# Optimization experiments

Hardware: AMD Instinct MI355X
Metric: run time of the kernel (lower is better)

The kernel has to match this reference:

```python
import jax, jax.numpy as jnp
import numpy as np

HIDDEN = 2048
KEY_DIM = 2048
NUM_HEADS = 16
HEAD_DIM = KEY_DIM // NUM_HEADS
ROPE_THETA = 10000.0
EPS = 1e-05


def rms_norm(x, w, eps=EPS):
    var = jnp.mean(x * x, axis=-1, keepdims=True)
    return x * jax.lax.rsqrt(var + eps) * w


def apply_rope(x, theta_base=ROPE_THETA):
    # x: [b, s, h, d]; faithful to the einops repeat '(2 d)' = tile (concat), with
    # even output positions = cos*x1 - sin*x2, odd = sin*x1 + cos*x2.
    b, s, h, d = x.shape
    half = d // 2
    freqs = theta_base ** (jnp.arange(half, dtype=x.dtype) * (-2.0 / d))  # [d/2]
    freqs = jnp.concatenate([freqs, freqs], axis=-1)                      # [d] (tiled)
    pos = jnp.arange(s, dtype=x.dtype)                                    # [s]
    ang = pos[:, None] * freqs[None, :]                                   # [s, d]
    cos = jnp.cos(ang)[None, :, None, :]
    sin = jnp.sin(ang)[None, :, None, :]
    x_even = x[..., 0::2]
    x_odd = x[..., 1::2]
    x1 = jnp.concatenate([x_even, x_even], axis=-1)  # tile '(2 d)'
    x2 = jnp.concatenate([x_odd, x_odd], axis=-1)
    even_mask = (jnp.arange(d) % 2 == 0)[None, None, None, :]
    return jnp.where(even_mask, cos * x1 - sin * x2, sin * x1 + cos * x2)


def setup_inputs() -> dict:
    key = jax.random.key(0)
    ks = jax.random.split(key, 10)
    B, S = 2, 2048
    s_in = 1.0 / np.sqrt(HIDDEN)
    s_k = 1.0 / np.sqrt(KEY_DIM)
    return {
        "x": jax.random.normal(ks[0], (B, S, HIDDEN), dtype=jnp.float32),
        "rms_w": jnp.ones((HIDDEN,), dtype=jnp.float32),
        "wq": jax.random.normal(ks[1], (HIDDEN, KEY_DIM), dtype=jnp.float32) * s_in,
        "bq": jnp.zeros((KEY_DIM,), dtype=jnp.float32),
        "wk": jax.random.normal(ks[2], (HIDDEN, KEY_DIM), dtype=jnp.float32) * s_in,
        "bk": jnp.zeros((KEY_DIM,), dtype=jnp.float32),
        "wv": jax.random.normal(ks[3], (HIDDEN, KEY_DIM), dtype=jnp.float32) * s_in,
        "bv": jnp.zeros((KEY_DIM,), dtype=jnp.float32),
        "wo": jax.random.normal(ks[4], (KEY_DIM, HIDDEN), dtype=jnp.float32) * s_k,
        "bo": jnp.zeros((HIDDEN,), dtype=jnp.float32),
    }


def reference(x, rms_w, wq, bq, wk, bk, wv, bv, wo, bo):
    B, S, _ = x.shape
    residual = x
    xn = rms_norm(x, rms_w)
    q = (xn @ wq + bq).reshape(B, S, NUM_HEADS, HEAD_DIM)
    k = (xn @ wk + bk).reshape(B, S, NUM_HEADS, HEAD_DIM)
    v = (xn @ wv + bv).reshape(B, S, NUM_HEADS, HEAD_DIM)
    q = apply_rope(q)
    k = apply_rope(k)
    scores = jnp.einsum('bshd,bthd->bhst', q, k) / jnp.sqrt(
        jnp.asarray(HEAD_DIM, dtype=x.dtype))
    causal = jnp.tril(jnp.ones((S, S), dtype=bool))[None, None]
    scores = jnp.where(causal, scores, -jnp.inf)
    probs = jax.nn.softmax(scores, axis=-1)
    out = jnp.einsum('bhst,bthd->bshd', probs, v).reshape(B, S, KEY_DIM)
    return out @ wo + bo + residual
```

## Files before the change

### kernel.cpp

```cpp
#include <hip/hip_runtime.h>
#include <stdint.h>
#include <math.h>

#define S_LEN 2048
#define HID 2048
#define NH 16
#define HD 128
#define NROWS 4096
#define SCALE 0.08838834764831845f
#define C2 (0.08838834764831845f * 1.442695040888963f)

typedef unsigned short u16;
typedef __attribute__((ext_vector_type(8))) short short8;
typedef __attribute__((ext_vector_type(4))) float f32x4;
typedef __attribute__((ext_vector_type(16))) float f32x16;
typedef __attribute__((ext_vector_type(4))) unsigned short u16x4;
typedef __attribute__((ext_vector_type(4))) unsigned int u32x4;
typedef __attribute__((ext_vector_type(4))) float float4v;

__device__ __forceinline__ u16 f2bf(float f) {
  union { float f; uint32_t u; } v; v.f = f;
  uint32_t r = v.u + 0x7FFFu + ((v.u >> 16) & 1u);
  return (u16)(r >> 16);
}
__device__ __forceinline__ float bf2f(u16 b) {
  union { uint32_t u; float f; } v; v.u = ((uint32_t)b) << 16;
  return v.f;
}
__device__ __forceinline__ void gl_lds16(const void* g, void* l) {
  __builtin_amdgcn_global_load_lds((const __attribute__((address_space(1))) void*)g,
                                   (__attribute__((address_space(3))) void*)l, 16, 0, 0);
}
__device__ __forceinline__ unsigned cvtpk(float lo, float hi) {
  unsigned r;
  asm("v_cvt_pk_bf16_f32 %0, %1, %2" : "=v"(r) : "v"(lo), "v"(hi));
  return r;
}
__device__ __forceinline__ void plswap(unsigned &a, unsigned &b) {
  asm volatile("v_permlane32_swap_b32 %0, %1" : "+v"(a), "+v"(b));
}

__global__ __launch_bounds__(256) void k_pre(const float* __restrict__ x, const float* __restrict__ rw,
                                             u16* __restrict__ xn,
                                             const float* __restrict__ w0, const float* __restrict__ w1,
                                             const float* __restrict__ w2, const float* __restrict__ w3,
                                             u16* __restrict__ wtbase) {
  int bid = blockIdx.x;
  int tid = threadIdx.x;
  if (bid < 4096) {
    int row = bid;
    const float* xr = x + (size_t)row * HID;
    float4v a = *(const float4v*)(xr + tid * 8);
    float4v b = *(const float4v*)(xr + tid * 8 + 4);
    float s = a[0]*a[0] + a[1]*a[1] + a[2]*a[2] + a[3]*a[3]
            + b[0]*b[0] + b[1]*b[1] + b[2]*b[2] + b[3]*b[3];
    #pragma unroll
    for (int off = 1; off < 64; off <<= 1) s += __shfl_xor(s, off, 64);
    __shared__ float red[4];
    int wv = tid >> 6;
    if ((tid & 63) == 0) red[wv] = s;
    __syncthreads();
    float tot = red[0] + red[1] + red[2] + red[3];
    float r = rsqrtf(tot * (1.0f / HID) + 1e-5f);
    const float* wp = rw + tid * 8;
    u16x4 o0, o1;
    #pragma unroll
    for (int j = 0; j < 4; ++j) { o0[j] = f2bf(a[j] * r * wp[j]); o1[j] = f2bf(b[j] * r * wp[4 + j]); }
    *(u16x4*)(xn + (size_t)row * HID + tid * 8) = o0;
    *(u16x4*)(xn + (size_t)row * HID + tid * 8 + 4) = o1;
  } else {
    int c = bid - 4096;
    int z = c >> 10;
    int rest = c & 1023;
    int n0 = (rest & 31) * 64, k0 = (rest >> 5) * 64;
    const float* w = (z == 0) ? w0 : (z == 1) ? w1 : (z == 2) ? w2 : w3;
    u16* wt = wtbase + (size_t)z * HID * HID;
    __shared__ float t[64][68];
    int cr = tid >> 4;
    int cc = (tid & 15) * 4;
    #pragma unroll
    for (int it = 0; it < 4; ++it) {
      int kk = cr + it * 16;
      float4v v = *(const float4v*)(w + (size_t)(k0 + kk) * HID + n0 + cc);
      t[kk][cc] = v[0]; t[kk][cc + 1] = v[1]; t[kk][cc + 2] = v[2]; t[kk][cc + 3] = v[3];
    }
    __syncthreads();
    #pragma unroll
    for (int it = 0; it < 4; ++it) {
      int nn = cr + it * 16;
      u16x4 o;
      #pragma unroll
      for (int j = 0; j < 4; ++j) o[j] = f2bf(t[cc + j][nn]);
      *(u16x4*)(wt + (size_t)(n0 + nn) * HID + k0 + cc) = o;
    }
  }
}

__global__ __launch_bounds__(256) void k_post(const u16* __restrict__ qh, const u16* __restrict__ kh,
                                              u16* __restrict__ QP, u16* __restrict__ KP,
                                              const u16* __restrict__ vh, u16* __restrict__ VP) {
  int bid = blockIdx.x;
  int tid = threadIdx.x;
  if (bid < 4096) {
    int l = tid & 63, wvv = tid >> 6;
    int rsub = l >> 4, c = l & 15;
    int row = bid * 16 + wvv * 4 + rsub;
    int bh = row >> 11, s = row & 2047;
    int tile = s >> 5, ln = s & 31;
    int ks = c >> 1, hi = c & 1;
    int k3 = ks & 3;
    const u16* qi = qh + (size_t)row * HD + 32 * k3 + 16 * hi;
    const u16* ki = kh + (size_t)row * HD + 32 * k3 + 16 * hi;
    float sn[8], cs[8];
    #pragma unroll
    for (int j = 0; j < 8; ++j) {
      int de = 16 * k3 + 8 * hi + j;
      float freq = exp2f((float)de * -0.20762050593046014f);
      sincosf((float)s * freq, &sn[j], &cs[j]);
    }
    size_t off = ((((size_t)(bh * 64 + tile)) * 8 + ks) * 64 + hi * 32 + ln) * 8;
    {
      short8 a = *(const short8*)(qi);
      short8 b2 = *(const short8*)(qi + 8);
      u16x4 o0, o1;
      #pragma unroll
      for (int j = 0; j < 4; ++j) {
        float x0 = bf2f((u16)a[2 * j]), x1 = bf2f((u16)a[2 * j + 1]);
        o0[j] = f2bf((j & 1) ? (sn[j] * x0 + cs[j] * x1) : (cs[j] * x0 - sn[j] * x1));
      }
      #pragma unroll
      for (int j = 0; j < 4; ++j) {
        int jj = j + 4;
        float x0 = bf2f((u16)b2[2 * j]), x1 = bf2f((u16)b2[2 * j + 1]);
        o1[j] = f2bf((jj & 1) ? (sn[jj] * x0 + cs[jj] * x1) : (cs[jj] * x0 - sn[jj] * x1));
      }
      *(u16x4*)(QP + off) = o0; *(u16x4*)(QP + off + 4) = o1;
    }
    {
      short8 a = *(const short8*)(ki);
      short8 b2 = *(const short8*)(ki + 8);
      u16x4 o0, o1;
      #pragma unroll
      for (int j = 0; j < 4; ++j) {
        float x0 = bf2f((u16)a[2 * j]), x1 = bf2f((u16)a[2 * j + 1]);
        o0[j] = f2bf((j & 1) ? (sn[j] * x0 + cs[j] * x1) : (cs[j] * x0 - sn[j] * x1));
      }
      #pragma unroll
      for (int j = 0; j < 4; ++j) {
        int jj = j + 4;
        float x0 = bf2f((u16)b2[2 * j]), x1 = bf2f((u16)b2[2 * j + 1]);
        o1[j] = f2bf((jj & 1) ? (sn[jj] * x0 + cs[jj] * x1) : (cs[jj] * x0 - sn[jj] * x1));
      }
      *(u16x4*)(KP + off) = o0; *(u16x4*)(KP + off + 4) = o1;
    }
  } else {
    int c = bid - 4096;
    int bx = c & 31;
    int bh = c >> 5;
    __shared__ u16 t[64][136];
    int row = tid >> 2;
    int d0 = (tid & 3) * 32;
    const u16* src = vh + ((size_t)bh * S_LEN + bx * 64 + row) * HD + d0;
    short8 a = *(const short8*)(src);
    short8 b = *(const short8*)(src + 8);
    short8 cc2 = *(const short8*)(src + 16);
    short8 d = *(const short8*)(src + 24);
    *(short8*)(&t[row][d0]) = a;
    *(short8*)(&t[row][d0 + 8]) = b;
    *(short8*)(&t[row][d0 + 16]) = cc2;
    *(short8*)(&t[row][d0 + 24]) = d;
    __syncthreads();
    #pragma unroll
    for (int i = 0; i < 4; ++i) {
      int cid = i * 256 + tid;
      int lp = cid & 63;
      int db = (cid >> 6) & 3;
      int j2 = (cid >> 8) & 1;
      int tl = (cid >> 9) & 1;
      int tg = bx * 2 + tl;
      int tloc = tl * 32 + j2 * 16 + (lp >> 5) * 8;
      int dloc = db * 32 + (lp & 31);
      short8 v;
      #pragma unroll
      for (int jj = 0; jj < 8; ++jj) v[jj] = (short)t[tloc + jj][dloc];
      size_t off = ((((size_t)(bh * 64 + tg) * 2 + j2) * 4 + db) * 64 + lp) * 8;
      *(short8*)(VP + off) = v;
    }
  }
}

__global__ __launch_bounds__(512, 1) void k_gemm_qkv2(const u16* __restrict__ A, const u16* __restrict__ BT,
                                                      const float* __restrict__ bq, const float* __restrict__ bk,
                                                      const float* __restrict__ bv, u16* __restrict__ qkv) {
  extern __shared__ __align__(16) char smraw[];
  u16* sm = (u16*)smraw;
  int bid = blockIdx.x;
  int xcd = bid & 7, loc = bid >> 3;
  int bx = xcd * 3 + loc % 3;
  int by = loc / 3;
  int tid = threadIdx.x;
  int w = tid >> 6, lane = tid & 63;
  int wr = w >> 2, wc = w & 3;
  int lq = lane & 15, lg = lane >> 4;

  f32x4 acc[4][4];
  #pragma unroll
  for (int mi = 0; mi < 4; ++mi)
    #pragma unroll
    for (int ni = 0; ni < 4; ++ni) acc[mi][ni] = (f32x4){0.f, 0.f, 0.f, 0.f};

  const size_t Abase = (size_t)(by * 128) * HID;
  const size_t Bbase = (size_t)(bx * 256) * HID;

  #define STAGE_A(n)  do { \
    int slot_ = ((n) % 3) * 24576; \
    int kb_ = (n) * 64; \
    _Pragma("unroll") \
    for (int it_ = 0; it_ < 2; ++it_) { \
      int c_ = it_ * 512 + tid; int row_ = c_ >> 3; int cs_ = (c_ & 7) ^ (row_ & 7); \
      gl_lds16(A + Abase + (size_t)row_ * HID + kb_ + cs_ * 8, sm + slot_ + c_ * 8); } \
  } while (0)
  #define STAGE_B(n, h)  do { \
    int slot_ = ((n) % 3) * 24576; \
    int kb_ = (n) * 64; \
    _Pragma("unroll") \
    for (int it_ = 0; it_ < 2; ++it_) { \
      int c_ = it_ * 512 + tid; int row_ = c_ >> 3; int cs_ = (c_ & 7) ^ (row_ & 7); \
      gl_lds16(BT + Bbase + (size_t)(128 * (h) + row_) * HID + kb_ + cs_ * 8, \
               sm + slot_ + 8192 + 8192 * (h) + c_ * 8); } \
  } while (0)

  STAGE_A(0); STAGE_B(0, 0); STAGE_B(0, 1);
  STAGE_A(1); STAGE_B(1, 0); STAGE_B(1, 1);
  asm volatile("s_waitcnt vmcnt(6)" ::: "memory");
  __builtin_amdgcn_s_barrier();
  __builtin_amdgcn_sched_barrier(0);

  for (int t = 0; t < 32; ++t) {
    int slot = (t % 3) * 24576;
    const u16* sA = sm + slot;
    const u16* sB = sm + slot + 8192;
    if (t == 31) asm volatile("s_waitcnt vmcnt(0)" ::: "memory");
    else         asm volatile("s_waitcnt vmcnt(6)" ::: "memory");
    short8 af[4][2], bf0[2][2];
    #pragma unroll
    for (int mi = 0; mi < 4; ++mi) {
      int ra = wr * 64 + mi * 16 + lq;
      #pragma unroll
      for (int ks = 0; ks < 2; ++ks)
        af[mi][ks] = *(const short8*)(sA + ra * 64 + (((ks * 4 + lg) ^ (ra & 7)) << 3));
    }
    #pragma unroll
    for (int nl = 0; nl < 2; ++nl) {
      int rb = wc * 64 + nl * 16 + lq;
      #pragma unroll
      for (int ks = 0; ks < 2; ++ks)
        bf0[nl][ks] = *(const short8*)(sB + rb * 64 + (((ks * 4 + lg) ^ (rb & 7)) << 3));
    }
    if (t + 2 < 32) { STAGE_A(t + 2); STAGE_B(t + 2, 0); }
    __builtin_amdgcn_s_setprio(1);
    #pragma unroll
    for (int ks = 0; ks < 2; ++ks)
      #pragma unroll
      for (int mi = 0; mi < 4; ++mi)
        #pragma unroll
        for (int nl = 0; nl < 2; ++nl)
          acc[mi][nl] = __builtin_amdgcn_mfma_f32_16x16x32_bf16(af[mi][ks], bf0[nl][ks], acc[mi][nl], 0, 0, 0);
    __builtin_amdgcn_s_setprio(0);
    __builtin_amdgcn_s_barrier();
    __builtin_amdgcn_sched_barrier(0);
    short8 bf1[2][2];
    #pragma unroll
    for (int nl = 0; nl < 2; ++nl) {
      int rb = wc * 64 + (nl + 2) * 16 + lq;
      #pragma unroll
      for (int ks = 0; ks < 2; ++ks)
        bf1[nl][ks] = *(const short8*)(sB + rb * 64 + (((ks * 4 + lg) ^ (rb & 7)) << 3));
    }
    if (t + 2 < 32) STAGE_B(t + 2, 1);
    __builtin_amdgcn_s_setprio(1);
    #pragma unroll
    for (int ks = 0; ks < 2; ++ks)
      #pragma unroll
      for (int mi = 0; mi < 4; ++mi)
        #pragma unroll
        for (int nl = 0; nl < 2; ++nl)
          acc[mi][nl + 2] = __builtin_amdgcn_mfma_f32_16x16x32_bf16(af[mi][ks], bf1[nl][ks], acc[mi][nl + 2], 0, 0, 0);
    __builtin_amdgcn_s_setprio(0);
    __builtin_amdgcn_s_barrier();
    __builtin_amdgcn_sched_barrier(0);
  }

  #pragma unroll
  for (int ni = 0; ni < 4; ++ni) {
    int colg = bx * 256 + wc * 64 + ni * 16 + lq;
    int sel = colg >> 11;
    int col = colg & 2047;
    int h = col >> 7, d = col & 127;
    const float* bias = (sel == 0) ? bq : (sel == 1) ? bk : bv;
    float bs = bias[col];
    u16* outp = qkv + (size_t)sel * NROWS * HID;
    #pragma unroll
    for (int mi = 0; mi < 4; ++mi) {
      #pragma unroll
      for (int r = 0; r < 4; ++r) {
        int rowm = by * 128 + wr * 64 + mi * 16 + lg * 4 + r;
        int b = rowm >> 11, s = rowm & 2047;
        outp[(((size_t)(b * NH + h)) * S_LEN + s) * HD + d] = f2bf(acc[mi][ni][r] + bs);
      }
    }
  }
  #undef STAGE_A
  #undef STAGE_B
}

__global__ __launch_bounds__(256, 3) void k_gemm_o2(const u16* __restrict__ A, const u16* __restrict__ BT,
                                                    const float* __restrict__ bias,
                                                    const float* __restrict__ resid,
                                                    float* __restrict__ outp) {
  extern __shared__ __align__(16) char smraw[];
  u16* sm = (u16*)smraw;
  int bid = blockIdx.x;
  int xcd = bid & 7, loc = bid >> 3;
  int bx = xcd * 2 + (loc & 1);
  int by = loc >> 1;
  int tid = threadIdx.x;
  int w = tid >> 6, lane = tid & 63;
  int wr = w >> 1, wc = w & 1;
  int lq = lane & 15, lg = lane >> 4;

  f32x4 acc[4][4];
  #pragma unroll
  for (int mi = 0; mi < 4; ++mi)
    #pragma unroll
    for (int ni = 0; ni < 4; ++ni) acc[mi][ni] = (f32x4){0.f, 0.f, 0.f, 0.f};

  const size_t Abase = (size_t)(by * 128) * HID;
  const size_t Bbase = (size_t)(bx * 128) * HID;

  #define STAGE_O(n)  do { \
    int slot_ = ((n) % 3) * 8192; \
    int kb_ = (n) * 32; \
    _Pragma("unroll") \
    for (int it_ = 0; it_ < 2; ++it_) { \
      int c_ = it_ * 256 + tid; int row_ = c_ >> 2; int ch_ = (c_ & 3) ^ ((row_ >> 1) & 3); \
      gl_lds16(A + Abase + (size_t)row_ * HID + kb_ + ch_ * 8, sm + slot_ + c_ * 8); } \
    _Pragma("unroll") \
    for (int it_ = 0; it_ < 2; ++it_) { \
      int c_ = it_ * 256 + tid; int row_ = c_ >> 2; int ch_ = (c_ & 3) ^ ((row_ >> 1) & 3); \
      gl_lds16(BT + Bbase + (size_t)row_ * HID + kb_ + ch_ * 8, sm + slot_ + 4096 + c_ * 8); } \
  } while (0)

  STAGE_O(0); STAGE_O(1);
  asm volatile("s_waitcnt vmcnt(4)" ::: "memory");
  __builtin_amdgcn_s_barrier();
  __builtin_amdgcn_sched_barrier(0);

  for (int n = 0; n < 64; ++n) {
    if (n + 2 <= 63) STAGE_O(n + 2);
    int slot = (n % 3) * 8192;
    const u16* sA = sm + slot;
    const u16* sB = sm + slot + 4096;
    short8 af[4], bf[4];
    #pragma unroll
    for (int mi = 0; mi < 4; ++mi) {
      int ra = wr * 64 + mi * 16 + lq;
      af[mi] = *(const short8*)(sA + ra * 32 + ((lg ^ ((ra >> 1) & 3)) << 3));
    }
    #pragma unroll
    for (int ni = 0; ni < 4; ++ni) {
      int rb = wc * 64 + ni * 16 + lq;
      bf[ni] = *(const short8*)(sB + rb * 32 + ((lg ^ ((rb >> 1) & 3)) << 3));
    }
    __builtin_amdgcn_s_setprio(1);
    #pragma unroll
    for (int mi = 0; mi < 4; ++mi)
      #pragma unroll
      for (int ni = 0; ni < 4; ++ni)
        acc[mi][ni] = __builtin_amdgcn_mfma_f32_16x16x32_bf16(af[mi], bf[ni], acc[mi][ni], 0, 0, 0);
    __builtin_amdgcn_s_setprio(0);
    if (n <= 61) {
      asm volatile("s_waitcnt vmcnt(4)" ::: "memory");
      __builtin_amdgcn_s_barrier();
      __builtin_amdgcn_sched_barrier(0);
    } else if (n == 62) {
      asm volatile("s_waitcnt vmcnt(0)" ::: "memory");
      __builtin_amdgcn_s_barrier();
      __builtin_amdgcn_sched_barrier(0);
    }
  }

  #pragma unroll
  for (int ni = 0; ni < 4; ++ni) {
    int col = bx * 128 + wc * 64 + ni * 16 + lq;
    float bs = bias[col];
    #pragma unroll
    for (int mi = 0; mi < 4; ++mi) {
      #pragma unroll
      for (int r = 0; r < 4; ++r) {
        int rowm = by * 128 + wr * 64 + mi * 16 + lg * 4 + r;
        size_t o = (size_t)rowm * HID + col;
        outp[o] = acc[mi][ni][r] + bs + resid[o];
      }
    }
  }
  #undef STAGE_O
}

__global__ __launch_bounds__(64, 2) void k_attn(const u16* __restrict__ QP, const u16* __restrict__ KP,
                                                const u16* __restrict__ VP, u16* __restrict__ out) {
  int bid = blockIdx.x;
  int rest = bid >> 3;
  int bh = (bid & 7) * 4 + (rest & 3);
  int gg = rest >> 2;
  int qw = (gg < 32) ? (63 - gg) : (gg - 32);
  int b = bh >> 4, h = bh & 15;
  int lane = threadIdx.x;
  int hi = lane >> 5, ln = lane & 31;
  int q0 = qw * 32, qrow = q0 + ln;

  const u16* QPb = QP + ((size_t)(bh * 64 + qw) * 8) * 512 + lane * 8;
  short8 qf[8];
  #pragma unroll
  for (int ks = 0; ks < 8; ++ks) qf[ks] = *(const short8*)(QPb + ks * 512);

  f32x16 oc[4];
  #pragma unroll
  for (int db = 0; db < 4; ++db)
    #pragma unroll
    for (int r = 0; r < 16; ++r) oc[db][r] = 0.f;
  float mr = -3.0e38f, l = 0.f;

  const u16* KPb = KP + ((size_t)bh * 64 * 8) * 512 + lane * 8;
  const u16* VPb = VP + ((size_t)bh * 64 * 8) * 512 + lane * 8;

  int ntile = qw + 1;
  short8 kf[8];
  #pragma unroll
  for (int ks = 0; ks < 8; ++ks) kf[ks] = *(const short8*)(KPb + ks * 512);

  for (int tt = 0; tt < ntile; ++tt) {
    short8 va[8];
    #pragma unroll
    for (int u = 0; u < 8; ++u) va[u] = *(const short8*)(VPb + (size_t)tt * 4096 + u * 512);

    f32x16 st;
    #pragma unroll
    for (int r = 0; r < 16; ++r) st[r] = 0.f;
    __builtin_amdgcn_s_setprio(1);
    #pragma unroll
    for (int ks = 0; ks < 8; ++ks)
      st = __builtin_amdgcn_mfma_f32_32x32x16_bf16(kf[ks], qf[ks], st, 0, 0, 0);
    __builtin_amdgcn_s_setprio(0);

    if (tt + 1 < ntile) {
      #pragma unroll
      for (int ks = 0; ks < 8; ++ks)
        kf[ks] = *(const short8*)(KPb + (size_t)(tt + 1) * 4096 + ks * 512);
    }

    int t0 = tt * 32;
    float sv[16];
    float pm = -3.0e38f;
    bool lastt = (tt == ntile - 1);
    #pragma unroll
    for (int r = 0; r < 16; ++r) {
      float x = st[r];
      if (lastt) {
        int t = t0 + (r & 3) + 8 * (r >> 2) + 4 * hi;
        x = (t <= qrow) ? x : -3.0e38f;
      }
      sv[r] = x;
    }
    #pragma unroll
    for (int r = 0; r < 15; r += 2) pm = fmaxf(fmaxf(pm, sv[r]), sv[r + 1]);
    pm = fmaxf(pm, sv[15]);
    pm = fmaxf(pm, __shfl_xor(pm, 32, 64));
    if (!__all(pm <= mr + 64.0f)) {
      float mnew = fmaxf(mr, pm);
      float al = exp2f((mr - mnew) * C2);
      l *= al;
      #pragma unroll
      for (int db = 0; db < 4; ++db)
        #pragma unroll
        for (int r = 0; r < 16; ++r) oc[db][r] *= al;
      mr = mnew;
    }
    float mc = mr * C2;
    float e[16];
    float rs = 0.f;
    #pragma unroll
    for (int r = 0; r < 16; ++r) {
      e[r] = exp2f(fmaf(sv[r], C2, -mc));
      rs += e[r];
    }
    rs += __shfl_xor(rs, 32, 64);
    l += rs;

    unsigned w0 = cvtpk(e[0], e[1]),   w1 = cvtpk(e[2], e[3]);
    unsigned w2 = cvtpk(e[4], e[5]),   w3 = cvtpk(e[6], e[7]);
    unsigned w4 = cvtpk(e[8], e[9]),   w5 = cvtpk(e[10], e[11]);
    unsigned w6 = cvtpk(e[12], e[13]), w7 = cvtpk(e[14], e[15]);
    plswap(w0, w2); plswap(w1, w3); plswap(w4, w6); plswap(w5, w7);
    u32x4 pw0 = {w0, w1, w2, w3};
    u32x4 pw1 = {w4, w5, w6, w7};
    short8 pb0 = __builtin_bit_cast(short8, pw0);
    short8 pb1 = __builtin_bit_cast(short8, pw1);

    __builtin_amdgcn_s_setprio(1);
    #pragma unroll
    for (int db = 0; db < 4; ++db)
      oc[db] = __builtin_amdgcn_mfma_f32_32x32x16_bf16(va[db], pb0, oc[db], 0, 0, 0);
    #pragma unroll
    for (int db = 0; db < 4; ++db)
      oc[db] = __builtin_amdgcn_mfma_f32_32x32x16_bf16(va[4 + db], pb1, oc[db], 0, 0, 0);
    __builtin_amdgcn_s_setprio(0);
  }

  float inv = 1.0f / l;
  size_t ob = ((size_t)(b * S_LEN + qrow)) * HID + h * HD;
  #pragma unroll
  for (int db = 0; db < 4; ++db) {
    #pragma unroll
    for (int g = 0; g < 4; ++g) {
      u16x4 pk;
      #pragma unroll
      for (int j = 0; j < 4; ++j) pk[j] = f2bf(oc[db][4 * g + j] * inv);
      *(u16x4*)(out + ob + db * 32 + 8 * g + 4 * hi) = pk;
    }
  }
}

extern "C" void kernel_launch(void* const* d_in, const int* in_sizes, int n_in,
                              void* d_out, int out_size, void* d_ws, size_t ws_size,
                              hipStream_t stream) {
  const float* x    = (const float*)d_in[0];
  const float* rmsw = (const float*)d_in[1];
  const float* wq   = (const float*)d_in[2];
  const float* bq   = (const float*)d_in[3];
  const float* wk   = (const float*)d_in[4];
  const float* bk   = (const float*)d_in[5];
  const float* wv   = (const float*)d_in[6];
  const float* bv   = (const float*)d_in[7];
  const float* wo   = (const float*)d_in[8];
  const float* bo   = (const float*)d_in[9];

  char* ws = (char*)d_ws;
  const size_t SZ = (size_t)NROWS * HID * 2;
  const size_t WSZ = (size_t)HID * HID * 2;
  u16* xn   = (u16*)(ws);
  u16* wqkT = (u16*)(ws + SZ);
  u16* woT  = (u16*)(ws + SZ + 3 * WSZ);
  u16* qhm  = (u16*)(ws + SZ + 4 * WSZ);
  u16* khm  = (u16*)(ws + SZ + 4 * WSZ + SZ);
  u16* vhm  = (u16*)(ws + SZ + 4 * WSZ + 2 * SZ);
  u16* QP   = xn;
  u16* KP   = wqkT;
  u16* VP   = khm;
  u16* ao   = qhm;

  k_pre<<<dim3(8192), dim3(256), 0, stream>>>(x, rmsw, xn, wq, wk, wv, wo, wqkT);
  k_gemm_qkv2<<<dim3(768), dim3(512), 147456, stream>>>(xn, wqkT, bq, bk, bv, qhm);
  k_post<<<dim3(5120), dim3(256), 0, stream>>>(qhm, khm, QP, KP, vhm, VP);
  k_attn<<<dim3(2048), dim3(64), 0, stream>>>(QP, KP, VP, ao);
  k_gemm_o2<<<dim3(512), dim3(256), 49152, stream>>>(ao, woT, bo, x, (float*)d_out);
}
```

Baseline: 255.2 us.

## Enlarge output-projection GEMM tile to 128x256 with 512 threads and split-phase pipeline

The output projection GEMM moves from 128x128 tiles with 256 threads and 512 blocks to 128x256 tiles with 512 threads (8 waves) and 256 blocks. Each K step now covers 64 elements, with an 8-way XOR LDS swizzle and a three-slot buffer of 144 KB. Each iteration is split into two halves over the N columns, and the next stage's global-to-LDS loads are interleaved between them. The aim is more operand reuse per LDS byte and fewer loop iterations. The cost is one block per CU, 256 blocks for the chip's CUs, and the removal of the XCD-aware block remapping.

```diff
diff --git a/kernel.cpp b/kernel.cpp
--- a/kernel.cpp
+++ b/kernel.cpp
@@ -314,19 +314,18 @@
   #undef STAGE_B
 }
 
-__global__ __launch_bounds__(256, 3) void k_gemm_o2(const u16* __restrict__ A, const u16* __restrict__ BT,
+__global__ __launch_bounds__(512, 1) void k_gemm_o2(const u16* __restrict__ A, const u16* __restrict__ BT,
                                                     const float* __restrict__ bias,
                                                     const float* __restrict__ resid,
                                                     float* __restrict__ outp) {
   extern __shared__ __align__(16) char smraw[];
   u16* sm = (u16*)smraw;
   int bid = blockIdx.x;
-  int xcd = bid & 7, loc = bid >> 3;
-  int bx = xcd * 2 + (loc & 1);
-  int by = loc >> 1;
+  int bx = bid & 7;
+  int by = bid >> 3;
   int tid = threadIdx.x;
   int w = tid >> 6, lane = tid & 63;
-  int wr = w >> 1, wc = w & 1;
+  int wr = w >> 2, wc = w & 3;
   int lq = lane & 15, lg = lane >> 4;
 
   f32x4 acc[4][4];
@@ -336,63 +335,90 @@
     for (int ni = 0; ni < 4; ++ni) acc[mi][ni] = (f32x4){0.f, 0.f, 0.f, 0.f};
 
   const size_t Abase = (size_t)(by * 128) * HID;
-  const size_t Bbase = (size_t)(bx * 128) * HID;
-
-  #define STAGE_O(n)  do { \
-    int slot_ = ((n) % 3) * 8192; \
-    int kb_ = (n) * 32; \
+  const size_t Bbase = (size_t)(bx * 256) * HID;
+
+  #define STAGE_A(n)  do { \
+    int slot_ = ((n) % 3) * 24576; \
+    int kb_ = (n) * 64; \
     _Pragma("unroll") \
     for (int it_ = 0; it_ < 2; ++it_) { \
-      int c_ = it_ * 256 + tid; int row_ = c_ >> 2; int ch_ = (c_ & 3) ^ ((row_ >> 1) & 3); \
-      gl_lds16(A + Abase + (size_t)row_ * HID + kb_ + ch_ * 8, sm + slot_ + c_ * 8); } \
+      int c_ = it_ * 512 + tid; int row_ = c_ >> 3; int cs_ = (c_ & 7) ^ (row_ & 7); \
+      gl_lds16(A + Abase + (size_t)row_ * HID + kb_ + cs_ * 8, sm + slot_ + c_ * 8); } \
+  } while (0)
+  #define STAGE_B(n, h)  do { \
+    int slot_ = ((n) % 3) * 24576; \
+    int kb_ = (n) * 64; \
     _Pragma("unroll") \
     for (int it_ = 0; it_ < 2; ++it_) { \
-      int c_ = it_ * 256 + tid; int row_ = c_ >> 2; int ch_ = (c_ & 3) ^ ((row_ >> 1) & 3); \
-      gl_lds16(BT + Bbase + (size_t)row_ * HID + kb_ + ch_ * 8, sm + slot_ + 4096 + c_ * 8); } \
+      int c_ = it_ * 512 + tid; int row_ = c_ >> 3; int cs_ = (c_ & 7) ^ (row_ & 7); \
+      gl_lds16(BT + Bbase + (size_t)(128 * (h) + row_) * HID + kb_ + cs_ * 8, \
+               sm + slot_ + 8192 + 8192 * (h) + c_ * 8); } \
   } while (0)
 
-  STAGE_O(0); STAGE_O(1);
-  asm volatile("s_waitcnt vmcnt(4)" ::: "memory");
+  STAGE_A(0); STAGE_B(0, 0); STAGE_B(0, 1);
+  STAGE_A(1); STAGE_B(1, 0); STAGE_B(1, 1);
+  asm volatile("s_waitcnt vmcnt(6)" ::: "memory");
   __builtin_amdgcn_s_barrier();
   __builtin_amdgcn_sched_barrier(0);
 
-  for (int n = 0; n < 64; ++n) {
-    if (n + 2 <= 63) STAGE_O(n + 2);
-    int slot = (n % 3) * 8192;
+  for (int t = 0; t < 32; ++t) {
+    int slot = (t % 3) * 24576;
     const u16* sA = sm + slot;
-    const u16* sB = sm + slot + 4096;
-    short8 af[4], bf[4];
+    const u16* sB = sm + slot + 8192;
+    if (t == 31) asm volatile("s_waitcnt vmcnt(0)" ::: "memory");
+    else         asm volatile("s_waitcnt vmcnt(6)" ::: "memory");
+    short8 af[4][2], bf0[2][2];
     #pragma unroll
     for (int mi = 0; mi < 4; ++mi) {
       int ra = wr * 64 + mi * 16 + lq;
-      af[mi] = *(const short8*)(sA + ra * 32 + ((lg ^ ((ra >> 1) & 3)) << 3));
-    }
-    #pragma unroll
-    for (int ni = 0; ni < 4; ++ni) {
-      int rb = wc * 64 + ni * 16 + lq;
-      bf[ni] = *(const short8*)(sB + rb * 32 + ((lg ^ ((rb >> 1) & 3)) << 3));
-    }
+      #pragma unroll
+      for (int ks = 0; ks < 2; ++ks)
+        af[mi][ks] = *(const short8*)(sA + ra * 64 + (((ks * 4 + lg) ^ (ra & 7)) << 3));
+    }
+    #pragma unroll
+    for (int nl = 0; nl < 2; ++nl) {
+      int rb = wc * 64 + nl * 16 + lq;
+      #pragma unroll
+      for (int ks = 0; ks < 2; ++ks)
+        bf0[nl][ks] = *(const short8*)(sB + rb * 64 + (((ks * 4 + lg) ^ (rb & 7)) << 3));
+    }
+    if (t + 2 < 32) { STAGE_A(t + 2); STAGE_B(t + 2, 0); }
     __builtin_amdgcn_s_setprio(1);
     #pragma unroll
-    for (int mi = 0; mi < 4; ++mi)
-      #pragma unroll
-      for (int ni = 0; ni < 4; ++ni)
-        acc[mi][ni] = __builtin_amdgcn_mfma_f32_16x16x32_bf16(af[mi], bf[ni], acc[mi][ni], 0, 0, 0);
+    for (int ks = 0; ks < 2; ++ks)
+      #pragma unroll
+      for (int mi = 0; mi < 4; ++mi)
+        #pragma unroll
+        for (int nl = 0; nl < 2; ++nl)
+          acc[mi][nl] = __builtin_amdgcn_mfma_f32_16x16x32_bf16(af[mi][ks], bf0[nl][ks], acc[mi][nl], 0, 0, 0);
     __builtin_amdgcn_s_setprio(0);
-    if (n <= 61) {
-      asm volatile("s_waitcnt vmcnt(4)" ::: "memory");
-      __builtin_amdgcn_s_barrier();
-      __builtin_amdgcn_sched_barrier(0);
-    } else if (n == 62) {
-      asm volatile("s_waitcnt vmcnt(0)" ::: "memory");
-      __builtin_amdgcn_s_barrier();
-      __builtin_amdgcn_sched_barrier(0);
-    }
+    __builtin_amdgcn_s_barrier();
+    __builtin_amdgcn_sched_barrier(0);
+    short8 bf1[2][2];
+    #pragma unroll
+    for (int nl = 0; nl < 2; ++nl) {
+      int rb = wc * 64 + (nl + 2) * 16 + lq;
+      #pragma unroll
+      for (int ks = 0; ks < 2; ++ks)
+        bf1[nl][ks] = *(const short8*)(sB + rb * 64 + (((ks * 4 + lg) ^ (rb & 7)) << 3));
+    }
+    if (t + 2 < 32) STAGE_B(t + 2, 1);
+    __builtin_amdgcn_s_setprio(1);
+    #pragma unroll
+    for (int ks = 0; ks < 2; ++ks)
+      #pragma unroll
+      for (int mi = 0; mi < 4; ++mi)
+        #pragma unroll
+        for (int nl = 0; nl < 2; ++nl)
+          acc[mi][nl + 2] = __builtin_amdgcn_mfma_f32_16x16x32_bf16(af[mi][ks], bf1[nl][ks], acc[mi][nl + 2], 0, 0, 0);
+    __builtin_amdgcn_s_setprio(0);
+    __builtin_amdgcn_s_barrier();
+    __builtin_amdgcn_sched_barrier(0);
   }
 
   #pragma unroll
   for (int ni = 0; ni < 4; ++ni) {
-    int col = bx * 128 + wc * 64 + ni * 16 + lq;
+    int col = bx * 256 + wc * 64 + ni * 16 + lq;
     float bs = bias[col];
     #pragma unroll
     for (int mi = 0; mi < 4; ++mi) {
@@ -404,7 +430,8 @@
       }
     }
   }
-  #undef STAGE_O
+  #undef STAGE_A
+  #undef STAGE_B
 }
 
 __global__ __launch_bounds__(64, 2) void k_attn(const u16* __restrict__ QP, const u16* __restrict__ KP,
@@ -563,5 +590,5 @@
   k_gemm_qkv2<<<dim3(768), dim3(512), 147456, stream>>>(xn, wqkT, bq, bk, bv, qhm);
   k_post<<<dim3(5120), dim3(256), 0, stream>>>(qhm, khm, QP, KP, vhm, VP);
   k_attn<<<dim3(2048), dim3(64), 0, stream>>>(QP, KP, VP, ao);
-  k_gemm_o2<<<dim3(512), dim3(256), 49152, stream>>>(ao, woT, bo, x, (float*)d_out);
-}
+  k_gemm_o2<<<dim3(256), dim3(512), 147456, stream>>>(ao, woT, bo, x, (float*)d_out);
+}
```

After: 243.9 us. 4.5% less time.
